# Kernel optimization log

Hardware: AMD Instinct MI355X
Metric: run time of the kernel (lower is better)

The kernel has to match this reference:

```python
import jax, jax.numpy as jnp
import numpy as np

N_SEG = 128      # number of ragged segments (len(leng))
TOTAL = 32768    # total rows = sum(leng)
D = 1280         # cnn_feature (tf_efficientnet_b0 classifier.in_features)
D_HEAD = 512     # hidden of logits head


def setup_inputs() -> dict:
    key = jax.random.key(0)
    ks = jax.random.split(key, 8)
    # ragged lengths (static at trace time), summing exactly to TOTAL
    rng = np.random.default_rng(0)
    leng = rng.integers(64, 448, size=N_SEG).astype(np.int64)
    leng = np.maximum((leng * (TOTAL / leng.sum())).astype(np.int64), 1)
    leng[-1] += TOTAL - leng.sum()
    segment_ids = jnp.asarray(np.repeat(np.arange(N_SEG), leng), jnp.int32)

    features = jax.random.normal(ks[0], (TOTAL, D), jnp.float32)
    s = 0.02
    Ww = jax.random.normal(ks[1], (D, D), jnp.float32) * s        # proj_w.weight
    bw = jnp.zeros((D,), jnp.float32)                              # proj_w.bias
    v = jax.random.normal(ks[2], (D,), jnp.float32) * s           # proj_v.weight (1,D) squeezed
    W1 = jax.random.normal(ks[3], (D_HEAD, D), jnp.float32) * s   # logits[0].weight
    b1 = jnp.zeros((D_HEAD,), jnp.float32)
    W2 = jax.random.normal(ks[4], (1, D_HEAD), jnp.float32) * s   # logits[3].weight
    b2 = jnp.zeros((1,), jnp.float32)
    return {"features": features, "Ww": Ww, "bw": bw, "v": v,
            "W1": W1, "b1": b1, "W2": W2, "b2": b2,
            "segment_ids": segment_ids}


def reference(features, Ww, bw, v, W1, b1, W2, b2, segment_ids):
    # per-row attention logits: tanh(x @ Ww^T + bw) @ v    -> [TOTAL]
    H = jnp.tanh(features @ Ww.T + bw)
    s = H @ v
    # segment-wise stable softmax (replaces Python loop over leng)
    m = jax.ops.segment_max(s, segment_ids, num_segments=N_SEG)
    e = jnp.exp(s - m[segment_ids])
    z = jax.ops.segment_sum(e, segment_ids, num_segments=N_SEG)
    att = e / z[segment_ids]                                      # [TOTAL]
    # attention-weighted sum pooling per segment -> [N_SEG, D]
    pooled = jax.ops.segment_sum(features * att[:, None], segment_ids,
                                 num_segments=N_SEG)
    # logits head (dropout is identity in eval)
    h = jax.nn.relu(pooled @ W1.T + b1)
    return h @ W2.T + b2                                          # [N_SEG, 1]
```

## Files before the change

### kernel.cpp

```cpp
#include <hip/hip_runtime.h>
#include <hip/hip_bf16.h>


#define TOTAL_ROWS 32768
#define DIM 1280
#define NSEG 128
#define DHEAD 512
#define NKT 20
#define NPART 4

typedef _Float16 f16x8 __attribute__((ext_vector_type(8)));
typedef _Float16 f16x4 __attribute__((ext_vector_type(4)));
typedef float f32x4 __attribute__((ext_vector_type(4)));

#define OFF_XH   0
#define OFF_WH   83886080
#define OFF_S    87162880
#define OFF_SEG  87425024
#define OFF_POOL 87426048
#define OFF_H    88081408
#define OFF_PP   OFF_WH

__device__ __forceinline__ void load_lds16(const void* g, void* l) {
  __builtin_amdgcn_global_load_lds(
      (const __attribute__((address_space(1))) unsigned int*)g,
      (__attribute__((address_space(3))) unsigned int*)l, 16, 0, 0);
}

__device__ __forceinline__ float tanh_fast(float x) {
  float e = __expf(2.0f * x);
  return 1.0f - 2.0f * __builtin_amdgcn_rcpf(e + 1.0f);
}

__global__ void cvt_init_kernel(const float* __restrict__ a, _Float16* __restrict__ oa,
                                int na8, const float* __restrict__ b,
                                _Float16* __restrict__ ob, int nb8,
                                const int* __restrict__ sid,
                                int* __restrict__ segstart, float* __restrict__ s) {
  int i = blockIdx.x * blockDim.x + threadIdx.x;
  if (i < TOTAL_ROWS) {
    s[i] = 0.f;
    int sg = sid[i];
    if (i == 0) segstart[0] = 0;
    else if (sid[i - 1] != sg) segstart[sg] = i;
    if (i == TOTAL_ROWS - 1) segstart[sg + 1] = TOTAL_ROWS;
  }
  const float* in;
  _Float16* out;
  int idx;
  if (i < na8) {
    in = a; out = oa; idx = i;
  } else {
    idx = i - na8;
    if (idx >= nb8) return;
    in = b; out = ob;
  }
  const float4* p = (const float4*)in + (size_t)idx * 2;
  float4 u0 = p[0], u1 = p[1];
  f16x8 h;
  h[0] = (_Float16)u0.x; h[1] = (_Float16)u0.y;
  h[2] = (_Float16)u0.z; h[3] = (_Float16)u0.w;
  h[4] = (_Float16)u1.x; h[5] = (_Float16)u1.y;
  h[6] = (_Float16)u1.z; h[7] = (_Float16)u1.w;
  *((f16x8*)out + idx) = h;
}

__global__ __launch_bounds__(512, 2) void gemm_s_kernel(
    const _Float16* __restrict__ X, const _Float16* __restrict__ W,
    const float* __restrict__ v, const float* __restrict__ bw,
    float* __restrict__ s) {
  __shared__ _Float16 As[2][2][8192];
  __shared__ _Float16 Bs[2][2][8192];

  const int rowBase = blockIdx.x * 256;
  const int jBase = blockIdx.y * 256;
  const int t = threadIdx.x;
  const int lane = t & 63;
  const int w = t >> 6;
  const int wm = w >> 2;
  const int wn = w & 3;
  const int lm = lane & 15;
  const int kc = lane >> 4;
  const int bh = wn >> 1;

  const int subrow = lane >> 3;
  const int g = ((lane & 7) - subrow) & 7;
  const _Float16* gA = X + (size_t)(rowBase + w * 8 + subrow) * DIM + g * 8;
  const _Float16* gB = W + (size_t)(jBase + w * 8 + subrow) * DIM + g * 8;

  int aOff[2], bOff[2];
#pragma unroll
  for (int ks = 0; ks < 2; ++ks) {
    int swz = ((ks * 4 + kc + lm) & 7) * 8;
    aOff[ks] = lm * 64 + swz;
    bOff[ks] = ((wn & 1) * 64 + lm) * 64 + swz;
  }

  f32x4 acc[8][4];
  const f32x4 zero = {0.f, 0.f, 0.f, 0.f};
#pragma unroll
  for (int i = 0; i < 8; ++i)
#pragma unroll
    for (int j = 0; j < 4; ++j) acc[i][j] = zero;

  f16x8 a[4][2], b[4][2];

#define STAGE_A(BUF, HALF, TT) do { \
    const _Float16* _src = gA + (size_t)(HALF) * 128 * DIM + (size_t)(TT) * 64; \
    load_lds16(_src, &As[BUF][HALF][w * 512]); \
    load_lds16(_src + 64 * DIM, &As[BUF][HALF][4096 + w * 512]); \
  } while (0)
#define STAGE_B(BUF, HALF, TT) do { \
    const _Float16* _src = gB + (size_t)(HALF) * 128 * DIM + (size_t)(TT) * 64; \
    load_lds16(_src, &Bs[BUF][HALF][w * 512]); \
    load_lds16(_src + 64 * DIM, &Bs[BUF][HALF][4096 + w * 512]); \
  } while (0)

#define PH_READ_A(BUF, MTB) do { \
    _Pragma("unroll") for (int mt = 0; mt < 4; ++mt) \
    _Pragma("unroll") for (int ks = 0; ks < 2; ++ks) \
      a[mt][ks] = *(const f16x8*)&As[BUF][wm][aOff[ks] + (MTB + mt) * 1024]; \
  } while (0)
#define PH_READ_B(BUF) do { \
    _Pragma("unroll") for (int nt = 0; nt < 4; ++nt) \
    _Pragma("unroll") for (int ks = 0; ks < 2; ++ks) \
      b[nt][ks] = *(const f16x8*)&Bs[BUF][bh][bOff[ks] + nt * 1024]; \
  } while (0)
#define PH_MFMA(MTB) do { \
    __builtin_amdgcn_s_setprio(1); \
    _Pragma("unroll") for (int mt = 0; mt < 4; ++mt) \
    _Pragma("unroll") for (int nt = 0; nt < 4; ++nt) \
    _Pragma("unroll") for (int ks = 0; ks < 2; ++ks) \
      acc[MTB + mt][nt] = __builtin_amdgcn_mfma_f32_16x16x32_f16( \
          a[mt][ks], b[nt][ks], acc[MTB + mt][nt], 0, 0, 0); \
    __builtin_amdgcn_s_setprio(0); \
  } while (0)

#define CFENCE asm volatile("" ::: "memory")
#define LGKM0  asm volatile("s_waitcnt lgkmcnt(0)" ::: "memory")
#define WAIT_VM4 asm volatile("s_waitcnt vmcnt(4)" ::: "memory")
#define WAIT_VM0 asm volatile("s_waitcnt vmcnt(0)" ::: "memory")
#define BAR __builtin_amdgcn_s_barrier()

#define KTILE(BUF, SA, SB, TAILWAIT) do { \
    CFENCE; \
     \
    PH_READ_A(BUF, 0); PH_READ_B(BUF); SA; \
    LGKM0; PH_MFMA(0); \
    BAR; \
     \
    PH_READ_A(BUF, 4); SB; \
    LGKM0; PH_MFMA(4); \
    TAILWAIT; BAR; \
  } while (0)

  STAGE_A(0, 0, 0); STAGE_A(0, 1, 0);
  STAGE_B(0, 0, 0); STAGE_B(0, 1, 0);
  STAGE_B(1, 0, 1); STAGE_B(1, 1, 1);
  WAIT_VM4;
  BAR;

  for (int kt = 0; kt < NKT - 2; kt += 2) {
    KTILE(0,
          { STAGE_A(1, 0, kt + 1); STAGE_A(1, 1, kt + 1); },
          { STAGE_B(0, 0, kt + 2); STAGE_B(0, 1, kt + 2); },
          WAIT_VM4);
    KTILE(1,
          { STAGE_A(0, 0, kt + 2); STAGE_A(0, 1, kt + 2); },
          { STAGE_B(1, 0, kt + 3); STAGE_B(1, 1, kt + 3); },
          WAIT_VM4);
  }
  KTILE(0,
        { STAGE_A(1, 0, NKT - 1); STAGE_A(1, 1, NKT - 1); },
        (void)0, WAIT_VM0);
  KTILE(1, (void)0, (void)0, (void)0);

#undef KTILE
#undef STAGE_A
#undef STAGE_B
#undef PH_READ_A
#undef PH_READ_B
#undef PH_MFMA

  const int colBase = jBase + wn * 64 + lm;
  float vv[4], bb[4];
#pragma unroll
  for (int nt = 0; nt < 4; ++nt) {
    int j = colBase + nt * 16;
    vv[nt] = v[j];
    bb[nt] = bw[j];
  }
  const int gq = lane >> 4;
#pragma unroll
  for (int mt = 0; mt < 8; ++mt) {
#pragma unroll
    for (int r = 0; r < 4; ++r) {
      float sumv = 0.f;
#pragma unroll
      for (int nt = 0; nt < 4; ++nt)
        sumv += tanh_fast(acc[mt][nt][r] + bb[nt]) * vv[nt];
      sumv += __shfl_xor(sumv, 1);
      sumv += __shfl_xor(sumv, 2);
      sumv += __shfl_xor(sumv, 4);
      sumv += __shfl_xor(sumv, 8);
      if (lm == 0) {
        int row = rowBase + wm * 128 + mt * 16 + gq * 4 + r;
        atomicAdd(&s[row], sumv);
      }
    }
  }
}

__global__ void softpool_kernel(const _Float16* __restrict__ F,
                                const float* __restrict__ s,
                                const int* __restrict__ segstart,
                                float* __restrict__ pooledp) {
  int seg = blockIdx.x, part = blockIdx.y;
  int st = segstart[seg], en = segstart[seg + 1];
  int t = threadIdx.x;
  __shared__ float redm[5], redz[5];
  float m = -1e30f;
  for (int i = st + t; i < en; i += 320) m = fmaxf(m, s[i]);
  for (int d = 1; d < 64; d <<= 1) m = fmaxf(m, __shfl_xor(m, d));
  if ((t & 63) == 0) redm[t >> 6] = m;
  __syncthreads();
  m = fmaxf(fmaxf(fmaxf(redm[0], redm[1]), fmaxf(redm[2], redm[3])), redm[4]);
  float z = 0.f;
  for (int i = st + t; i < en; i += 320) z += __expf(s[i] - m);
  for (int d = 1; d < 64; d <<= 1) z += __shfl_xor(z, d);
  if ((t & 63) == 0) redz[t >> 6] = z;
  __syncthreads();
  z = redz[0] + redz[1] + redz[2] + redz[3] + redz[4];
  float rz = 1.0f / z;

  int len = en - st;
  int chunk = (len + NPART - 1) / NPART;
  int r0 = st + chunk * part;
  int r1 = min(en, r0 + chunk);
  float acc[4] = {0.f, 0.f, 0.f, 0.f};
  int r = r0;
  for (; r + 2 <= r1; r += 2) {
    float a0 = __expf(s[r] - m) * rz;
    float a1 = __expf(s[r + 1] - m) * rz;
    f16x4 f0 = ((const f16x4*)(F + (size_t)r * DIM))[t];
    f16x4 f1 = ((const f16x4*)(F + (size_t)(r + 1) * DIM))[t];
#pragma unroll
    for (int c = 0; c < 4; ++c) {
      acc[c] = fmaf(a0, (float)f0[c], acc[c]);
      acc[c] = fmaf(a1, (float)f1[c], acc[c]);
    }
  }
  if (r < r1) {
    float a0 = __expf(s[r] - m) * rz;
    f16x4 f0 = ((const f16x4*)(F + (size_t)r * DIM))[t];
#pragma unroll
    for (int c = 0; c < 4; ++c) acc[c] = fmaf(a0, (float)f0[c], acc[c]);
  }
  float4 o;
  o.x = acc[0]; o.y = acc[1]; o.z = acc[2]; o.w = acc[3];
  *(float4*)(pooledp + ((size_t)part * NSEG + seg) * DIM + t * 4) = o;
}

__global__ void fold_kernel(const float* __restrict__ pp,
                            float* __restrict__ pooled) {
  int i = blockIdx.x * 256 + threadIdx.x;
  pooled[i] = pp[i] + pp[i + NSEG * DIM] + pp[i + 2 * NSEG * DIM] +
              pp[i + 3 * NSEG * DIM];
}

__global__ void head1_kernel(const float* __restrict__ pooled,
                             const float* __restrict__ W1,
                             const float* __restrict__ b1, float* __restrict__ h) {
  int og = blockIdx.x, sg = blockIdx.y;
  __shared__ float Wt[16 * 65];
  __shared__ float Pt[32 * 65];
  int t = threadIdx.x;
  int tx = t & 15, ty = t >> 4;
  float acc0 = 0.f, acc1 = 0.f;
  for (int kcc = 0; kcc < 20; ++kcc) {
    __syncthreads();
#pragma unroll
    for (int u = 0; u < 4; ++u) {
      int lin = t + 256 * u;
      int o = lin >> 6, kk = lin & 63;
      Wt[o * 65 + kk] = W1[(size_t)(og * 16 + o) * DIM + kcc * 64 + kk];
    }
#pragma unroll
    for (int u = 0; u < 8; ++u) {
      int lin = t + 256 * u;
      int ss = lin >> 6, kk = lin & 63;
      Pt[ss * 65 + kk] = pooled[(size_t)(sg * 32 + ss) * DIM + kcc * 64 + kk];
    }
    __syncthreads();
#pragma unroll
    for (int kk = 0; kk < 64; ++kk) {
      float wv = Wt[tx * 65 + kk];
      acc0 = fmaf(Pt[ty * 65 + kk], wv, acc0);
      acc1 = fmaf(Pt[(ty + 16) * 65 + kk], wv, acc1);
    }
  }
  int o = og * 16 + tx;
  float bias = b1[o];
  h[(size_t)(sg * 32 + ty) * DHEAD + o] = fmaxf(acc0 + bias, 0.f);
  h[(size_t)(sg * 32 + ty + 16) * DHEAD + o] = fmaxf(acc1 + bias, 0.f);
}

__global__ void head2_kernel(const float* __restrict__ h,
                             const float* __restrict__ W2,
                             const float* __restrict__ b2, float* __restrict__ out) {
  int seg = blockIdx.x;
  int t = threadIdx.x;
  float val = h[(size_t)seg * DHEAD + t] * W2[t] +
              h[(size_t)seg * DHEAD + t + 256] * W2[t + 256];
  for (int d = 1; d < 64; d <<= 1) val += __shfl_xor(val, d);
  __shared__ float red[4];
  if ((t & 63) == 0) red[t >> 6] = val;
  __syncthreads();
  if (t == 0) out[seg] = red[0] + red[1] + red[2] + red[3] + b2[0];
}

extern "C" void kernel_launch(void* const* d_in, const int* in_sizes, int n_in,
                              void* d_out, int out_size, void* d_ws, size_t ws_size,
                              hipStream_t stream) {
  const float* features = (const float*)d_in[0];
  const float* Ww = (const float*)d_in[1];
  const float* bw = (const float*)d_in[2];
  const float* v = (const float*)d_in[3];
  const float* W1 = (const float*)d_in[4];
  const float* b1 = (const float*)d_in[5];
  const float* W2 = (const float*)d_in[6];
  const float* b2 = (const float*)d_in[7];
  const int* segids = (const int*)d_in[8];
  float* out = (float*)d_out;

  char* ws = (char*)d_ws;
  _Float16* Xh = (_Float16*)(ws + OFF_XH);
  _Float16* Wh = (_Float16*)(ws + OFF_WH);
  float* s = (float*)(ws + OFF_S);
  int* segstart = (int*)(ws + OFF_SEG);
  float* pooled = (float*)(ws + OFF_POOL);
  float* pooledp = (float*)(ws + OFF_PP);
  float* h = (float*)(ws + OFF_H);

  const int na8 = TOTAL_ROWS * DIM / 8;
  const int nb8 = DIM * DIM / 8;
  cvt_init_kernel<<<(na8 + nb8 + 255) / 256, 256, 0, stream>>>(
      features, Xh, na8, Ww, Wh, nb8, segids, segstart, s);

  dim3 ggrid(TOTAL_ROWS / 256, DIM / 256);
  gemm_s_kernel<<<ggrid, 512, 0, stream>>>(Xh, Wh, v, bw, s);

  softpool_kernel<<<dim3(NSEG, NPART), 320, 0, stream>>>(Xh, s, segstart, pooledp);
  fold_kernel<<<NSEG * DIM / 256, 256, 0, stream>>>(pooledp, pooled);
  head1_kernel<<<dim3(32, 4), 256, 0, stream>>>(pooled, W1, b1, h);
  head2_kernel<<<NSEG, 256, 0, stream>>>(h, W2, b2, out);
}
```

Before: 463.1 us.

## Restructure GEMM k-tile into interleaved LDS-read/MFMA quads with one barrier

The two-phase k-tile, which had a lgkmcnt(0) wait and a barrier mid-tile, becomes a fine-grained sequence of small LDS reads interleaved with 2x2 MFMA quads. This lets the compiler overlap LDS latency with matrix work and leaves one barrier per tile. The A and B global-to-LDS prefetches are now issued together at the start of each tile with a full vmcnt(0) wait at the end. This replaces the earlier staggered schedule where B ran one tile further ahead, so the prefetch distance is shorter and global load latency may be less well hidden.

```diff
diff --git a/kernel.cpp b/kernel.cpp
--- a/kernel.cpp
+++ b/kernel.cpp
@@ -116,71 +116,81 @@
     load_lds16(_src + 64 * DIM, &Bs[BUF][HALF][4096 + w * 512]); \
   } while (0)
 
-#define PH_READ_A(BUF, MTB) do { \
-    _Pragma("unroll") for (int mt = 0; mt < 4; ++mt) \
+#define READ_A1(BUF, SLOT, MT) do { \
     _Pragma("unroll") for (int ks = 0; ks < 2; ++ks) \
-      a[mt][ks] = *(const f16x8*)&As[BUF][wm][aOff[ks] + (MTB + mt) * 1024]; \
-  } while (0)
-#define PH_READ_B(BUF) do { \
-    _Pragma("unroll") for (int nt = 0; nt < 4; ++nt) \
+      a[SLOT][ks] = *(const f16x8*)&As[BUF][wm][aOff[ks] + (MT) * 1024]; \
+  } while (0)
+#define READ_B1(BUF, NT) do { \
     _Pragma("unroll") for (int ks = 0; ks < 2; ++ks) \
-      b[nt][ks] = *(const f16x8*)&Bs[BUF][bh][bOff[ks] + nt * 1024]; \
-  } while (0)
-#define PH_MFMA(MTB) do { \
+      b[NT][ks] = *(const f16x8*)&Bs[BUF][bh][bOff[ks] + (NT) * 1024]; \
+  } while (0)
+#define MFMA_Q(S0, S1, R0, R1, N0, N1) do { \
     __builtin_amdgcn_s_setprio(1); \
-    _Pragma("unroll") for (int mt = 0; mt < 4; ++mt) \
-    _Pragma("unroll") for (int nt = 0; nt < 4; ++nt) \
-    _Pragma("unroll") for (int ks = 0; ks < 2; ++ks) \
-      acc[MTB + mt][nt] = __builtin_amdgcn_mfma_f32_16x16x32_f16( \
-          a[mt][ks], b[nt][ks], acc[MTB + mt][nt], 0, 0, 0); \
+    _Pragma("unroll") for (int ks = 0; ks < 2; ++ks) { \
+      acc[R0][N0] = __builtin_amdgcn_mfma_f32_16x16x32_f16( \
+          a[S0][ks], b[N0][ks], acc[R0][N0], 0, 0, 0); \
+      acc[R0][N1] = __builtin_amdgcn_mfma_f32_16x16x32_f16( \
+          a[S0][ks], b[N1][ks], acc[R0][N1], 0, 0, 0); \
+      acc[R1][N0] = __builtin_amdgcn_mfma_f32_16x16x32_f16( \
+          a[S1][ks], b[N0][ks], acc[R1][N0], 0, 0, 0); \
+      acc[R1][N1] = __builtin_amdgcn_mfma_f32_16x16x32_f16( \
+          a[S1][ks], b[N1][ks], acc[R1][N1], 0, 0, 0); \
+    } \
     __builtin_amdgcn_s_setprio(0); \
   } while (0)
 
 #define CFENCE asm volatile("" ::: "memory")
-#define LGKM0  asm volatile("s_waitcnt lgkmcnt(0)" ::: "memory")
-#define WAIT_VM4 asm volatile("s_waitcnt vmcnt(4)" ::: "memory")
 #define WAIT_VM0 asm volatile("s_waitcnt vmcnt(0)" ::: "memory")
 #define BAR __builtin_amdgcn_s_barrier()
+#define SCHED0 __builtin_amdgcn_sched_barrier(0)
 
 #define KTILE(BUF, SA, SB, TAILWAIT) do { \
     CFENCE; \
-     \
-    PH_READ_A(BUF, 0); PH_READ_B(BUF); SA; \
-    LGKM0; PH_MFMA(0); \
-    BAR; \
-     \
-    PH_READ_A(BUF, 4); SB; \
-    LGKM0; PH_MFMA(4); \
-    TAILWAIT; BAR; \
+    SA; SB; \
+    READ_B1(BUF, 0); READ_B1(BUF, 1); \
+    READ_A1(BUF, 0, 0); READ_A1(BUF, 1, 1); \
+    MFMA_Q(0, 1, 0, 1, 0, 1); \
+    READ_B1(BUF, 2); READ_B1(BUF, 3); \
+    MFMA_Q(0, 1, 0, 1, 2, 3); \
+    READ_A1(BUF, 2, 2); READ_A1(BUF, 3, 3); \
+    MFMA_Q(2, 3, 2, 3, 0, 1); \
+    MFMA_Q(2, 3, 2, 3, 2, 3); \
+    READ_A1(BUF, 0, 4); READ_A1(BUF, 1, 5); \
+    MFMA_Q(0, 1, 4, 5, 0, 1); \
+    MFMA_Q(0, 1, 4, 5, 2, 3); \
+    READ_A1(BUF, 2, 6); READ_A1(BUF, 3, 7); \
+    MFMA_Q(2, 3, 6, 7, 0, 1); \
+    MFMA_Q(2, 3, 6, 7, 2, 3); \
+    TAILWAIT; SCHED0; BAR; \
   } while (0)
 
   STAGE_A(0, 0, 0); STAGE_A(0, 1, 0);
   STAGE_B(0, 0, 0); STAGE_B(0, 1, 0);
-  STAGE_B(1, 0, 1); STAGE_B(1, 1, 1);
-  WAIT_VM4;
+  WAIT_VM0;
   BAR;
 
   for (int kt = 0; kt < NKT - 2; kt += 2) {
     KTILE(0,
           { STAGE_A(1, 0, kt + 1); STAGE_A(1, 1, kt + 1); },
-          { STAGE_B(0, 0, kt + 2); STAGE_B(0, 1, kt + 2); },
-          WAIT_VM4);
+          { STAGE_B(1, 0, kt + 1); STAGE_B(1, 1, kt + 1); },
+          WAIT_VM0);
     KTILE(1,
           { STAGE_A(0, 0, kt + 2); STAGE_A(0, 1, kt + 2); },
-          { STAGE_B(1, 0, kt + 3); STAGE_B(1, 1, kt + 3); },
-          WAIT_VM4);
+          { STAGE_B(0, 0, kt + 2); STAGE_B(0, 1, kt + 2); },
+          WAIT_VM0);
   }
   KTILE(0,
         { STAGE_A(1, 0, NKT - 1); STAGE_A(1, 1, NKT - 1); },
-        (void)0, WAIT_VM0);
+        { STAGE_B(1, 0, NKT - 1); STAGE_B(1, 1, NKT - 1); },
+        WAIT_VM0);
   KTILE(1, (void)0, (void)0, (void)0);
 
 #undef KTILE
 #undef STAGE_A
 #undef STAGE_B
-#undef PH_READ_A
-#undef PH_READ_B
-#undef PH_MFMA
+#undef READ_A1
+#undef READ_B1
+#undef MFMA_Q
 
   const int colBase = jBase + wn * 64 + lm;
   float vv[4], bb[4];
```

New measurement: 463.3 us. Within noise of the previous version (+0.0%).
